# Performance work log

Hardware: AMD Instinct MI355X
Metric: run time of the kernel (lower is better)

## Reference

```python
import jax, jax.numpy as jnp
import numpy as np


def setup_inputs() -> dict:
    key = jax.random.key(0)
    ks = jax.random.split(key, 6)
    B, T, U = 4, 160, 80
    De, Dd = 640, 640
    inner, vocab = 640, 1024
    return {
        "enc_state": jax.random.normal(ks[0], (B, T, De), jnp.float32),
        "dec_state": jax.random.normal(ks[1], (B, U, Dd), jnp.float32),
        "W1": jax.random.normal(ks[2], (De + Dd, inner), jnp.float32) * (1.0 / np.sqrt(De + Dd)),
        "b1": jax.random.normal(ks[3], (inner,), jnp.float32) * 0.02,
        "W2": jax.random.normal(ks[4], (inner, vocab), jnp.float32) * (1.0 / np.sqrt(inner)),
        "b2": jax.random.normal(ks[5], (vocab,), jnp.float32) * 0.02,
    }


def reference(enc_state, dec_state, W1, b1, W2, b2):
    # Faithful to: cat([enc tiled over U, dec tiled over T], -1) @ W1 + b1,
    # algebraically split so the [B,T,U,2D] concat is never materialized:
    # cat(e, d) @ W1 == e @ W1[:De] + d @ W1[De:]
    De = enc_state.shape[-1]
    W1_enc, W1_dec = W1[:De], W1[De:]
    enc_proj = jnp.einsum("btd,dh->bth", enc_state, W1_enc)   # [B,T,H]
    dec_proj = jnp.einsum("bud,dh->buh", dec_state, W1_dec)   # [B,U,H]
    # broadcast add over the (T,U) lattice -> [B,T,U,H]
    hidden = jnp.tanh(enc_proj[:, :, None, :] + dec_proj[:, None, :, :] + b1)
    logits = jnp.einsum("btuh,hv->btuv", hidden, W2) + b2     # [B,T,U,V]
    return logits
```

## Files before the change

### kernel.cpp

```cpp
#include <hip/hip_runtime.h>
#include <hip/hip_bf16.h>
#include <cstdint>

#define D_    640
#define V_    1024
#define M_    51200

typedef __bf16 bf16x8 __attribute__((ext_vector_type(8)));
typedef float floatx4 __attribute__((ext_vector_type(4)));

__device__ __forceinline__ void g2l16(const void* g, void* l) {
    __builtin_amdgcn_global_load_lds((const __attribute__((address_space(1))) void*)g,
                                     (__attribute__((address_space(3))) void*)l,
                                     16, 0, 0);
}

__device__ __forceinline__ float fast_tanh(float x) {
    float e = __builtin_amdgcn_exp2f(x * 2.8853900817779268f);
    return 1.0f - 2.0f * __builtin_amdgcn_rcpf(e + 1.0f);
}

__global__ __launch_bounds__(256) void proj_kernel(
    const float* __restrict__ enc, const float* __restrict__ dec,
    const float* __restrict__ W1, const float* __restrict__ b1,
    float* __restrict__ encp, float* __restrict__ decp) {
    __shared__ float As[64][36];
    __shared__ float Ws[32][68];

    const int rt = blockIdx.y;
    const int ct = blockIdx.x;
    const bool is_enc = (rt < 10);
    const float* Asrc; const float* Wsrc; float* Cdst;
    if (is_enc) { Asrc = enc + (size_t)rt * 64 * D_;        Wsrc = W1;           Cdst = encp + (size_t)rt * 64 * D_; }
    else        { Asrc = dec + (size_t)(rt - 10) * 64 * D_; Wsrc = W1 + D_ * D_; Cdst = decp + (size_t)(rt - 10) * 64 * D_; }

    const int tid = threadIdx.x;
    const int ar = tid >> 2,  ac = (tid & 3) * 8;
    const int wr2 = tid >> 3, wc2 = (tid & 7) * 8;
    const int tr = tid >> 4,  tc = tid & 15;

    float acc[4][4] = {};
    for (int k0 = 0; k0 < D_; k0 += 32) {
        __syncthreads();
        *(floatx4*)&As[ar][ac]       = *(const floatx4*)&Asrc[(size_t)ar * D_ + k0 + ac];
        *(floatx4*)&As[ar][ac + 4]   = *(const floatx4*)&Asrc[(size_t)ar * D_ + k0 + ac + 4];
        *(floatx4*)&Ws[wr2][wc2]     = *(const floatx4*)&Wsrc[(size_t)(k0 + wr2) * D_ + ct * 64 + wc2];
        *(floatx4*)&Ws[wr2][wc2 + 4] = *(const floatx4*)&Wsrc[(size_t)(k0 + wr2) * D_ + ct * 64 + wc2 + 4];
        __syncthreads();
#pragma unroll
        for (int kk = 0; kk < 32; kk++) {
            floatx4 w = *(const floatx4*)&Ws[kk][tc * 4];
            float a0 = As[tr * 4 + 0][kk], a1 = As[tr * 4 + 1][kk];
            float a2 = As[tr * 4 + 2][kk], a3 = As[tr * 4 + 3][kk];
#pragma unroll
            for (int j = 0; j < 4; j++) {
                acc[0][j] += a0 * w[j]; acc[1][j] += a1 * w[j];
                acc[2][j] += a2 * w[j]; acc[3][j] += a3 * w[j];
            }
        }
    }
    floatx4 bv = {0.f, 0.f, 0.f, 0.f};
    if (is_enc) bv = *(const floatx4*)&b1[ct * 64 + tc * 4];
#pragma unroll
    for (int i = 0; i < 4; i++) {
        floatx4 v = { acc[i][0] + bv[0], acc[i][1] + bv[1],
                      acc[i][2] + bv[2], acc[i][3] + bv[3] };
        *(floatx4*)&Cdst[(size_t)(tr * 4 + i) * D_ + ct * 64 + tc * 4] = v;
    }
}

__global__ __launch_bounds__(256) void w2t_kernel(
    const float* __restrict__ W2, __bf16* __restrict__ W2t) {
    __shared__ __bf16 tile[32][33];
    const int vt = blockIdx.x;
    const int kt = blockIdx.y;
    const int tx = threadIdx.x & 31, ty = threadIdx.x >> 5;
#pragma unroll
    for (int i = 0; i < 4; i++)
        tile[ty + i * 8][tx] = (__bf16)W2[(size_t)(kt * 32 + ty + i * 8) * V_ + vt * 32 + tx];
    __syncthreads();
#pragma unroll
    for (int i = 0; i < 4; i++)
        W2t[(size_t)(vt * 32 + ty + i * 8) * D_ + kt * 32 + tx] = tile[tx][ty + i * 8];
}

__global__ __launch_bounds__(256) void hidden_kernel(
    const float* __restrict__ encp, const float* __restrict__ decp,
    __bf16* __restrict__ H) {
    const unsigned g = blockIdx.x * 256u + threadIdx.x;
    const unsigned row = g / 80u;
    const unsigned hg  = g % 80u;
    const unsigned u   = row % 80u;
    const unsigned bt  = row / 80u;
    const unsigned b   = bt / 160u;

    const float* ep = encp + (size_t)bt * D_ + hg * 8;
    const float* dp = decp + (size_t)(b * 80u + u) * D_ + hg * 8;

    floatx4 e0 = *(const floatx4*)ep, e1 = *(const floatx4*)(ep + 4);
    floatx4 d0 = *(const floatx4*)dp, d1 = *(const floatx4*)(dp + 4);

    bf16x8 hv;
#pragma unroll
    for (int i = 0; i < 4; i++) hv[i]     = (__bf16)fast_tanh(e0[i] + d0[i]);
#pragma unroll
    for (int i = 0; i < 4; i++) hv[i + 4] = (__bf16)fast_tanh(e1[i] + d1[i]);

    *(bf16x8*)(H + (size_t)g * 8) = hv;
}

#define VM6  asm volatile("s_waitcnt vmcnt(6)" ::: "memory")
#define VM0  asm volatile("s_waitcnt vmcnt(0)" ::: "memory")
#define BAR  __builtin_amdgcn_s_barrier()
#define SCB  __builtin_amdgcn_sched_barrier(0)

#define STG_A(BUF, S, TL) do { \
    g2l16(Hb + (unsigned)((S)*163840 + (TL)*128) + agl,         ldsp + (BUF)*32768 + (S)*16384 + stl); \
    g2l16(Hb + (unsigned)((S)*163840 + (TL)*128 + 10240) + agl, ldsp + (BUF)*32768 + (S)*16384 + stl + 1024); \
  } while (0)
#define STG_B(BUF, S, TL) do { \
    g2l16(Wb + (unsigned)((S)*163840 + (TL)*128) + agl,         ldsp + 65536 + (BUF)*32768 + (S)*16384 + stl); \
    g2l16(Wb + (unsigned)((S)*163840 + (TL)*128 + 10240) + agl, ldsp + 65536 + (BUF)*32768 + (S)*16384 + stl + 1024); \
  } while (0)

#define RD_A(ABUF, QM) do { \
    _Pragma("unroll") for (int ii = 0; ii < 4; ++ii) { \
      af0[ii] = *(const bf16x8*)(ldsp + (ABUF)*32768 + (QM)*16384 + ii*2048 + aRowB + sx0); \
      af1[ii] = *(const bf16x8*)(ldsp + (ABUF)*32768 + (QM)*16384 + ii*2048 + aRowB + sx1); \
    } } while (0)
#define RD_B(BBUF, QN) do { \
    _Pragma("unroll") for (int jj = 0; jj < 2; ++jj) { \
      bg0[jj] = *(const bf16x8*)(ldsp + 65536 + (BBUF)*32768 + (QN)*16384 + jj*2048 + bRowB + sx0); \
      bg1[jj] = *(const bf16x8*)(ldsp + 65536 + (BBUF)*32768 + (QN)*16384 + jj*2048 + bRowB + sx1); \
    } } while (0)
#define MM(QM, QN) do { \
    __builtin_amdgcn_s_setprio(1); \
    _Pragma("unroll") for (int ii = 0; ii < 4; ++ii) \
      _Pragma("unroll") for (int jj = 0; jj < 2; ++jj) { \
        acc[(QM)*4+ii][(QN)*2+jj] = __builtin_amdgcn_mfma_f32_16x16x32_bf16(af0[ii], bg0[jj], acc[(QM)*4+ii][(QN)*2+jj], 0, 0, 0); \
        acc[(QM)*4+ii][(QN)*2+jj] = __builtin_amdgcn_mfma_f32_16x16x32_bf16(af1[ii], bg1[jj], acc[(QM)*4+ii][(QN)*2+jj], 0, 0, 0); \
      } \
    __builtin_amdgcn_s_setprio(0); \
  } while (0)

__global__ __launch_bounds__(512, 2) void gemm_kernel(
    const __bf16* __restrict__ H, const __bf16* __restrict__ W2t,
    const float* __restrict__ b2, float* __restrict__ C) {
    __shared__ __align__(128) char lds[131072];

    const int bid = blockIdx.x;
    const int swz = (bid & 7) * 100 + (bid >> 3);
    const int mt = swz >> 2, nt = swz & 3;
    const int m0 = mt * 256, n0 = nt * 256;

    const int tid = threadIdx.x;
    const int w = tid >> 6, l = tid & 63;
    const int wr = w >> 2, wc = w & 3;
    const int lrow = l & 15, lk = l >> 4, l7 = l & 7, lhi = l >> 3;

    const unsigned swzb = (unsigned)(((l & 7) ^ lhi) * 16);
    const unsigned agl  = (unsigned)((w * 16 + lhi) * 1280) + swzb;
    const unsigned stl  = (unsigned)(w * 2048 + l * 16);

    const char* Hb = (const char*)H   + (size_t)m0 * 1280;
    const char* Wb = (const char*)W2t + (size_t)n0 * 1280;
    char* ldsp = (char*)lds;

    const unsigned aRowB = (unsigned)((wr * 64 + lrow) * 128);
    const unsigned bRowB = (unsigned)(wc * 4096 + lrow * 128);
    const unsigned sx0 = (unsigned)(((0 + lk) ^ l7) * 16);
    const unsigned sx1 = (unsigned)(((4 + lk) ^ l7) * 16);

    floatx4 acc[8][4] = {};

    STG_A(0, 0, 0); STG_B(0, 0, 0); STG_A(0, 1, 0); STG_B(0, 1, 0);
    STG_B(1, 0, 1); STG_A(1, 1, 1); STG_B(1, 1, 1);
    VM6; BAR; SCB;

#pragma unroll 1
    for (int it = 0; it < 5; ++it) {
        const int t1 = 2 * it + 1, t2 = 2 * it + 2, t3 = 2 * it + 3;
        const bool g = (it < 4);
        bf16x8 af0[4], af1[4], bg0[2], bg1[2];

        RD_A(0, 0); RD_B(0, 0);
        STG_A(1, 0, t1);
        BAR; SCB; MM(0, 0); BAR; SCB;

        RD_A(0, 1);
        if (g) STG_B(0, 0, t2);
        BAR; SCB; MM(1, 0); BAR; SCB;

        RD_B(0, 1);
        if (g) STG_A(0, 1, t2);
        BAR; SCB; MM(1, 1); BAR; SCB;

        RD_A(0, 0);
        if (g) STG_B(0, 1, t2);
        if (it == 4) { VM0; } else { VM6; }
        BAR; SCB; MM(0, 1); BAR; SCB;

        RD_A(1, 0); RD_B(1, 0);
        if (g) STG_A(0, 0, t2);
        BAR; SCB; MM(0, 0); BAR; SCB;

        RD_A(1, 1);
        if (g) STG_B(1, 0, t3);
        BAR; SCB; MM(1, 0); BAR; SCB;

        RD_B(1, 1);
        if (g) STG_A(1, 1, t3);
        BAR; SCB; MM(1, 1); BAR; SCB;

        RD_A(1, 0);
        if (g) STG_B(1, 1, t3);
        if (g) { VM6; }
        BAR; SCB; MM(0, 1); BAR; SCB;
    }

#pragma unroll
    for (int j = 0; j < 4; ++j) {
        const int col = n0 + (j >> 1) * 128 + wc * 32 + (j & 1) * 16 + lrow;
        const float bj = b2[col];
#pragma unroll
        for (int i = 0; i < 8; ++i) {
            const int row = m0 + (i >> 2) * 128 + wr * 64 + (i & 3) * 16 + lk * 4;
            float* Cp = C + (size_t)row * V_ + col;
#pragma unroll
            for (int rg = 0; rg < 4; ++rg)
                Cp[(size_t)rg * V_] = acc[i][j][rg] + bj;
        }
    }
}

extern "C" void kernel_launch(void* const* d_in, const int* in_sizes, int n_in,
                              void* d_out, int out_size, void* d_ws, size_t ws_size,
                              hipStream_t stream) {
    const float* enc = (const float*)d_in[0];
    const float* dec = (const float*)d_in[1];
    const float* W1  = (const float*)d_in[2];
    const float* b1  = (const float*)d_in[3];
    const float* W2  = (const float*)d_in[4];
    const float* b2  = (const float*)d_in[5];
    float* out = (float*)d_out;

    char* ws = (char*)d_ws;
    float*  encp = (float*)ws;
    float*  decp = (float*)(ws + 1638400);
    __bf16* W2t  = (__bf16*)(ws + 1638400 + 819200);
    __bf16* Hbuf = (__bf16*)(ws + 1638400 + 819200 + 1310720);

    proj_kernel<<<dim3(10, 15), 256, 0, stream>>>(enc, dec, W1, b1, encp, decp);
    w2t_kernel<<<dim3(32, 20), 256, 0, stream>>>(W2, W2t);
    hidden_kernel<<<16000, 256, 0, stream>>>(encp, decp, Hbuf);
    gemm_kernel<<<800, 512, 0, stream>>>(Hbuf, W2t, b2, out);
}
```

Baseline: 352.4 us.

## Double-buffer MFMA register fragments to overlap LDS reads with matrix math

Splits the per-stage A/B register fragments into two ping-pong sets so the LDS reads for the next quadrant are issued before the MFMAs of the current quadrant, within the same barrier window. The first fragments are prefetched before the loop and the next iteration's are loaded at the end of each iteration. Launch bounds drop from 2 to 1 blocks per CU because the extra fragment registers raise register pressure. This trades occupancy for better in-wave latency hiding, and the reordered barriers must still protect the buffers being restaged.

```diff
diff --git a/kernel.cpp b/kernel.cpp
--- a/kernel.cpp
+++ b/kernel.cpp
@@ -123,27 +123,27 @@
     g2l16(Wb + (unsigned)((S)*163840 + (TL)*128 + 10240) + agl, ldsp + 65536 + (BUF)*32768 + (S)*16384 + stl + 1024); \
   } while (0)
 
-#define RD_A(ABUF, QM) do { \
+#define RD_A2(D0, D1, ABUF, QM) do { \
     _Pragma("unroll") for (int ii = 0; ii < 4; ++ii) { \
-      af0[ii] = *(const bf16x8*)(ldsp + (ABUF)*32768 + (QM)*16384 + ii*2048 + aRowB + sx0); \
-      af1[ii] = *(const bf16x8*)(ldsp + (ABUF)*32768 + (QM)*16384 + ii*2048 + aRowB + sx1); \
+      D0[ii] = *(const bf16x8*)(ldsp + (ABUF)*32768 + (QM)*16384 + ii*2048 + aRowB + sx0); \
+      D1[ii] = *(const bf16x8*)(ldsp + (ABUF)*32768 + (QM)*16384 + ii*2048 + aRowB + sx1); \
     } } while (0)
-#define RD_B(BBUF, QN) do { \
+#define RD_B2(G0, G1, BBUF, QN) do { \
     _Pragma("unroll") for (int jj = 0; jj < 2; ++jj) { \
-      bg0[jj] = *(const bf16x8*)(ldsp + 65536 + (BBUF)*32768 + (QN)*16384 + jj*2048 + bRowB + sx0); \
-      bg1[jj] = *(const bf16x8*)(ldsp + 65536 + (BBUF)*32768 + (QN)*16384 + jj*2048 + bRowB + sx1); \
+      G0[jj] = *(const bf16x8*)(ldsp + 65536 + (BBUF)*32768 + (QN)*16384 + jj*2048 + bRowB + sx0); \
+      G1[jj] = *(const bf16x8*)(ldsp + 65536 + (BBUF)*32768 + (QN)*16384 + jj*2048 + bRowB + sx1); \
     } } while (0)
-#define MM(QM, QN) do { \
+#define MM2(A0, A1, G0, G1, QM, QN) do { \
     __builtin_amdgcn_s_setprio(1); \
     _Pragma("unroll") for (int ii = 0; ii < 4; ++ii) \
       _Pragma("unroll") for (int jj = 0; jj < 2; ++jj) { \
-        acc[(QM)*4+ii][(QN)*2+jj] = __builtin_amdgcn_mfma_f32_16x16x32_bf16(af0[ii], bg0[jj], acc[(QM)*4+ii][(QN)*2+jj], 0, 0, 0); \
-        acc[(QM)*4+ii][(QN)*2+jj] = __builtin_amdgcn_mfma_f32_16x16x32_bf16(af1[ii], bg1[jj], acc[(QM)*4+ii][(QN)*2+jj], 0, 0, 0); \
+        acc[(QM)*4+ii][(QN)*2+jj] = __builtin_amdgcn_mfma_f32_16x16x32_bf16(A0[ii], G0[jj], acc[(QM)*4+ii][(QN)*2+jj], 0, 0, 0); \
+        acc[(QM)*4+ii][(QN)*2+jj] = __builtin_amdgcn_mfma_f32_16x16x32_bf16(A1[ii], G1[jj], acc[(QM)*4+ii][(QN)*2+jj], 0, 0, 0); \
       } \
     __builtin_amdgcn_s_setprio(0); \
   } while (0)
 
-__global__ __launch_bounds__(512, 2) void gemm_kernel(
+__global__ __launch_bounds__(512, 1) void gemm_kernel(
     const __bf16* __restrict__ H, const __bf16* __restrict__ W2t,
     const float* __restrict__ b2, float* __restrict__ C) {
     __shared__ __align__(128) char lds[131072];
@@ -172,50 +172,61 @@
     const unsigned sx1 = (unsigned)(((4 + lk) ^ l7) * 16);
 
     floatx4 acc[8][4] = {};
+    bf16x8 afX0[4], afX1[4], afY0[4], afY1[4];
+    bf16x8 bgX0[2], bgX1[2], bgY0[2], bgY1[2];
 
     STG_A(0, 0, 0); STG_B(0, 0, 0); STG_A(0, 1, 0); STG_B(0, 1, 0);
     STG_B(1, 0, 1); STG_A(1, 1, 1); STG_B(1, 1, 1);
     VM6; BAR; SCB;
+    RD_A2(afX0, afX1, 0, 0); RD_B2(bgX0, bgX1, 0, 0);
 
 #pragma unroll 1
     for (int it = 0; it < 5; ++it) {
         const int t1 = 2 * it + 1, t2 = 2 * it + 2, t3 = 2 * it + 3;
         const bool g = (it < 4);
-        bf16x8 af0[4], af1[4], bg0[2], bg1[2];
-
-        RD_A(0, 0); RD_B(0, 0);
+
         STG_A(1, 0, t1);
-        BAR; SCB; MM(0, 0); BAR; SCB;
-
-        RD_A(0, 1);
+        BAR; SCB;
+        RD_A2(afY0, afY1, 0, 1);
+        MM2(afX0, afX1, bgX0, bgX1, 0, 0);
+        BAR; SCB;
         if (g) STG_B(0, 0, t2);
-        BAR; SCB; MM(1, 0); BAR; SCB;
-
-        RD_B(0, 1);
+        BAR; SCB;
+        RD_B2(bgY0, bgY1, 0, 1);
+        MM2(afY0, afY1, bgX0, bgX1, 1, 0);
+        BAR; SCB;
         if (g) STG_A(0, 1, t2);
-        BAR; SCB; MM(1, 1); BAR; SCB;
-
-        RD_A(0, 0);
+        BAR; SCB;
+        MM2(afY0, afY1, bgY0, bgY1, 1, 1);
+        BAR; SCB;
         if (g) STG_B(0, 1, t2);
         if (it == 4) { VM0; } else { VM6; }
-        BAR; SCB; MM(0, 1); BAR; SCB;
-
-        RD_A(1, 0); RD_B(1, 0);
+        BAR; SCB;
+        RD_A2(afY0, afY1, 1, 0);
+        RD_B2(bgX0, bgX1, 1, 0);
+        MM2(afX0, afX1, bgY0, bgY1, 0, 1);
+        BAR; SCB;
+
         if (g) STG_A(0, 0, t2);
-        BAR; SCB; MM(0, 0); BAR; SCB;
-
-        RD_A(1, 1);
+        BAR; SCB;
+        RD_A2(afX0, afX1, 1, 1);
+        MM2(afY0, afY1, bgX0, bgX1, 0, 0);
+        BAR; SCB;
         if (g) STG_B(1, 0, t3);
-        BAR; SCB; MM(1, 0); BAR; SCB;
-
-        RD_B(1, 1);
+        BAR; SCB;
+        RD_B2(bgY0, bgY1, 1, 1);
+        MM2(afX0, afX1, bgX0, bgX1, 1, 0);
+        BAR; SCB;
         if (g) STG_A(1, 1, t3);
-        BAR; SCB; MM(1, 1); BAR; SCB;
-
-        RD_A(1, 0);
+        BAR; SCB;
+        MM2(afX0, afX1, bgY0, bgY1, 1, 1);
+        BAR; SCB;
         if (g) STG_B(1, 1, t3);
         if (g) { VM6; }
-        BAR; SCB; MM(0, 1); BAR; SCB;
+        BAR; SCB;
+        if (g) { RD_A2(afX0, afX1, 0, 0); RD_B2(bgX0, bgX1, 0, 0); }
+        MM2(afY0, afY1, bgY0, bgY1, 0, 1);
+        BAR; SCB;
     }
 
 #pragma unroll
```

New measurement: 347.8 us. About the same (-1.3%).
